# Kernel tuning notes

Hardware: AMD Instinct MI355X
Metric: run time of the kernel (lower is better)

The kernel has to match this reference:

```python
import jax, jax.numpy as jnp
import numpy as np

B, T, F, H = 1024, 128, 64, 256
HH = H // 2
A = 2  # action_space_size


def setup_inputs() -> dict:
    key = jax.random.key(0)
    ks = jax.random.split(key, 16)
    s = 0.05
    return {
        "history": jax.random.normal(ks[0], (B, T, F), jnp.float32),
        "head": jax.random.normal(ks[1], (B, 3), jnp.float32),
        # peephole LSTM params (TF LSTMCell gate order: i, j, f, o)
        "kernel": jax.random.normal(ks[2], (F + H, 4 * H), jnp.float32) * s,
        "bias": jnp.zeros((4 * H,), jnp.float32),
        "w_i": jax.random.normal(ks[3], (H,), jnp.float32) * s,
        "w_f": jax.random.normal(ks[4], (H,), jnp.float32) * s,
        "w_o": jax.random.normal(ks[5], (H,), jnp.float32) * s,
        # dueling heads
        "fc3_w": jax.random.normal(ks[6], (H + 2, HH), jnp.float32) * s,
        "fc3_b": jnp.zeros((HH,), jnp.float32),
        "fc4_w": jax.random.normal(ks[7], (H + 2, HH), jnp.float32) * s,
        "fc4_b": jnp.zeros((HH,), jnp.float32),
        "sell_v_w": jax.random.normal(ks[8], (HH, 1), jnp.float32) * s,
        "sell_v_b": jnp.zeros((1,), jnp.float32),
        "sell_q_w": jax.random.normal(ks[9], (HH, A), jnp.float32) * s,
        "sell_q_b": jnp.zeros((A,), jnp.float32),
        "buy_v_w": jax.random.normal(ks[10], (HH, 1), jnp.float32) * s,
        "buy_v_b": jnp.zeros((1,), jnp.float32),
        "buy_q_w": jax.random.normal(ks[11], (HH, A), jnp.float32) * s,
        "buy_q_b": jnp.zeros((A,), jnp.float32),
    }


def _peephole_lstm(history, kernel, bias, w_i, w_f, w_o):
    # history: [B, T, F] -> final hidden state h: [B, H]
    b = history.shape[0]
    h_dim = w_i.shape[0]
    xs = jnp.swapaxes(history, 0, 1)  # [T, B, F] time-major for scan
    c0 = jnp.zeros((b, h_dim), history.dtype)
    h0 = jnp.zeros((b, h_dim), history.dtype)

    def step(carry, x_t):
        c, h = carry
        z = jnp.concatenate([x_t, h], axis=-1) @ kernel + bias  # [B, 4H]
        i, j, f, o = jnp.split(z, 4, axis=-1)
        i = jax.nn.sigmoid(i + w_i * c)
        f = jax.nn.sigmoid(f + 1.0 + w_f * c)  # forget_bias = 1.0 (TF default)
        c_new = f * c + i * jnp.tanh(j)
        o = jax.nn.sigmoid(o + w_o * c_new)
        h_new = o * jnp.tanh(c_new)
        return (c_new, h_new), None

    (c_fin, h_fin), _ = jax.lax.scan(step, (c0, h0), xs)
    return h_fin


def reference(history, head, kernel, bias, w_i, w_f, w_o,
              fc3_w, fc3_b, fc4_w, fc4_b,
              sell_v_w, sell_v_b, sell_q_w, sell_q_b,
              buy_v_w, buy_v_b, buy_q_w, buy_q_b):
    state = _peephole_lstm(history, kernel, bias, w_i, w_f, w_o)  # [B, H]
    is_pos = head[:, :1]   # [B, 1]
    net_pnl = head[:, 1:]  # [B, 2]
    feature = jnp.concatenate([net_pnl, state], axis=-1)  # [B, H+2]

    value_logits = jax.nn.relu(feature @ fc3_w + fc3_b)
    q_logits = jax.nn.relu(feature @ fc4_w + fc4_b)

    pos_adv = q_logits @ sell_q_w + sell_q_b
    pos_q = pos_adv - jnp.mean(pos_adv, axis=-1, keepdims=True) + (value_logits @ sell_v_w + sell_v_b)
    emp_adv = q_logits @ buy_q_w + buy_q_b
    emp_q = emp_adv - jnp.mean(emp_adv, axis=-1, keepdims=True) + (value_logits @ buy_v_w + buy_v_b)

    mask = jnp.concatenate([is_pos, 1.0 - is_pos], axis=1).astype(bool)  # [B, 2]
    q = jnp.where(mask, pos_q, emp_q)
    return q
```

## Files before the change

kernel.cpp:

```cpp
#include <hip/hip_runtime.h>
#include <stdint.h>

#define B_TOTAL 1024
#define T_STEPS 128
#define F_DIM   64
#define H_DIM   256
#define BROWS   16
#define APAD    324
#define NSLOTS  640

typedef float f32x4 __attribute__((ext_vector_type(4)));
typedef short bf16x8 __attribute__((ext_vector_type(8)));

__device__ __forceinline__ unsigned short f2bf(float f) {
  unsigned int u = __float_as_uint(f);
  u += 0x7fffu + ((u >> 16) & 1u);
  return (unsigned short)(u >> 16);
}
__device__ __forceinline__ float bf2f(unsigned short b) {
  return __uint_as_float(((unsigned int)b) << 16);
}
__device__ __forceinline__ float sigmoid_f(float x) {
  return 1.0f / (1.0f + __expf(-x));
}
__device__ __forceinline__ float tanh_f(float x) {
  return 1.0f - 2.0f / (1.0f + __expf(2.0f * x));
}

__global__ __launch_bounds__(64) void pack_w_kernel(const float* __restrict__ W,
                                                    unsigned short* __restrict__ Wp) {
  const int slot = blockIdx.x;
  const int w  = slot / 80, r = slot % 80;
  const int kt = r >> 3, ct = (r >> 2) & 1, g = r & 3;
  const int ntile = g * 16 + w * 2 + ct;
  const int l   = threadIdx.x;
  const int col = ntile * 16 + (l & 15);
  const int k0  = kt * 32 + (l >> 4) * 8;
  unsigned short* dst = Wp + ((size_t)slot * 64 + l) * 8;
  #pragma unroll
  for (int j = 0; j < 8; ++j)
    dst[j] = f2bf(W[(size_t)(k0 + j) * 1024 + col]);
}

#define PIN(x) asm volatile("" : "+v"(x))

#define ISSUE_BATCH(buf, kt, ct) do {                                        \
    const unsigned short* _p = wp_wl + ((kt) * 8 + (ct) * 4) * 512;          \
    asm volatile("global_load_dwordx4 %0, %4, off\n\t"                       \
                 "global_load_dwordx4 %1, %4, off offset:1024\n\t"           \
                 "global_load_dwordx4 %2, %4, off offset:2048\n\t"           \
                 "global_load_dwordx4 %3, %4, off offset:3072"               \
                 : "=&v"(buf[0]), "=&v"(buf[1]), "=&v"(buf[2]), "=&v"(buf[3])\
                 : "v"(_p));                                                 \
  } while (0)

#define CONSUME(buf, ct, N) do {                                             \
    asm volatile("s_waitcnt vmcnt(" #N ")" ::: "memory");                    \
    __builtin_amdgcn_sched_barrier(0);                                       \
    acc[ct][0] = __builtin_amdgcn_mfma_f32_16x16x32_bf16(af, buf[0], acc[ct][0], 0, 0, 0); \
    acc[ct][1] = __builtin_amdgcn_mfma_f32_16x16x32_bf16(af, buf[1], acc[ct][1], 0, 0, 0); \
    acc[ct][2] = __builtin_amdgcn_mfma_f32_16x16x32_bf16(af, buf[2], acc[ct][2], 0, 0, 0); \
    acc[ct][3] = __builtin_amdgcn_mfma_f32_16x16x32_bf16(af, buf[3], acc[ct][3], 0, 0, 0); \
  } while (0)

#define LD_A(kt) (*(const bf16x8*)&A_lds[cl][(kt) * 32 + kg * 8])

__global__ __launch_bounds__(512, 1) void qlstm_kernel(
    const float* __restrict__ history, const float* __restrict__ head,
    const float* __restrict__ bias,
    const float* __restrict__ w_i, const float* __restrict__ w_f, const float* __restrict__ w_o,
    const unsigned short* __restrict__ Wp,
    const float* __restrict__ fc3_w, const float* __restrict__ fc3_b,
    const float* __restrict__ fc4_w, const float* __restrict__ fc4_b,
    const float* __restrict__ sell_v_w, const float* __restrict__ sell_v_b,
    const float* __restrict__ sell_q_w, const float* __restrict__ sell_q_b,
    const float* __restrict__ buy_v_w, const float* __restrict__ buy_v_b,
    const float* __restrict__ buy_q_w, const float* __restrict__ buy_q_b,
    float* __restrict__ out) {

  __shared__ unsigned short A_lds[BROWS][APAD];
  __shared__ float feat[BROWS][258];
  __shared__ float v_lds[BROWS][128];
  __shared__ float q_lds[BROWS][128];
  __shared__ float ispos_lds[BROWS];

  const int tid = threadIdx.x;
  const int w   = tid >> 6;
  const int l   = tid & 63;
  const int cl  = l & 15;
  const int kg  = l >> 4;
  const int rb  = blockIdx.x * BROWS;

  const unsigned short* wp_wl = Wp + (size_t)(w * 80) * 512 + l * 8;

  bf16x8 wreg[3][2][4];
  #pragma unroll
  for (int kt = 0; kt < 3; ++kt)
    #pragma unroll
    for (int ct = 0; ct < 2; ++ct)
      #pragma unroll
      for (int g = 0; g < 4; ++g) {
        wreg[kt][ct][g] = *(const bf16x8*)(wp_wl + (kt * 8 + ct * 4 + g) * 512);
        PIN(wreg[kt][ct][g]);
      }

  for (int i = tid; i < BROWS * APAD; i += 512)
    ((unsigned short*)A_lds)[i] = 0;
  __syncthreads();
  {
    const int r  = tid >> 5;
    const int f0 = (tid & 31) * 2;
    const float2 xv = *(const float2*)&history[((size_t)(rb + r) * T_STEPS + 0) * F_DIM + f0];
    *(unsigned int*)&A_lds[r][f0] =
        (unsigned int)f2bf(xv.x) | ((unsigned int)f2bf(xv.y) << 16);
  }

  float bias_r[2][4], wi_r[2], wf_r[2], wo_r[2];
  #pragma unroll
  for (int ct = 0; ct < 2; ++ct) {
    const int hc = (w * 2 + ct) * 16 + cl;
    wi_r[ct] = w_i[hc]; wf_r[ct] = w_f[hc]; wo_r[ct] = w_o[hc];
    #pragma unroll
    for (int g = 0; g < 4; ++g) bias_r[ct][g] = bias[g * 256 + hc];
  }

  float c_st[2][4];
  #pragma unroll
  for (int ct = 0; ct < 2; ++ct)
    #pragma unroll
    for (int q = 0; q < 4; ++q) c_st[ct][q] = 0.0f;

  __syncthreads();

  for (int t = 0; t < T_STEPS; ++t) {
    f32x4 acc[2][4];
    #pragma unroll
    for (int ct = 0; ct < 2; ++ct)
      #pragma unroll
      for (int g = 0; g < 4; ++g)
        acc[ct][g] = (f32x4){0.f, 0.f, 0.f, 0.f};

    float2 xv;
    const bool havex = (t + 1 < T_STEPS);
    if (havex) {
      const float* xp =
          &history[((size_t)(rb + (tid >> 5)) * T_STEPS + (t + 1)) * F_DIM + (tid & 31) * 2];
      asm volatile("global_load_dwordx2 %0, %1, off" : "=&v"(xv) : "v"(xp));
    }

    bf16x8 sA[4], sB[4], sC[4];
    ISSUE_BATCH(sA, 3, 0);
    ISSUE_BATCH(sB, 3, 1);
    ISSUE_BATCH(sC, 4, 0);

    #pragma unroll
    for (int kt = 0; kt < 3; ++kt) {
      const bf16x8 afr = LD_A(kt);
      #pragma unroll
      for (int ct = 0; ct < 2; ++ct)
        #pragma unroll
        for (int g = 0; g < 4; ++g)
          acc[ct][g] =
              __builtin_amdgcn_mfma_f32_16x16x32_bf16(afr, wreg[kt][ct][g], acc[ct][g], 0, 0, 0);
    }

    bf16x8 af;
    af = LD_A(3);
    CONSUME(sA, 0, 8); ISSUE_BATCH(sA, 4, 1);
    CONSUME(sB, 1, 8); ISSUE_BATCH(sB, 5, 0);
    af = LD_A(4);
    CONSUME(sC, 0, 8); ISSUE_BATCH(sC, 5, 1);
    CONSUME(sA, 1, 8); ISSUE_BATCH(sA, 6, 0);
    af = LD_A(5);
    CONSUME(sB, 0, 8); ISSUE_BATCH(sB, 6, 1);
    CONSUME(sC, 1, 8); ISSUE_BATCH(sC, 7, 0);
    af = LD_A(6);
    CONSUME(sA, 0, 8); ISSUE_BATCH(sA, 7, 1);
    CONSUME(sB, 1, 8); ISSUE_BATCH(sB, 8, 0);
    af = LD_A(7);
    CONSUME(sC, 0, 8); ISSUE_BATCH(sC, 8, 1);
    CONSUME(sA, 1, 8); ISSUE_BATCH(sA, 9, 0);
    af = LD_A(8);
    CONSUME(sB, 0, 8); ISSUE_BATCH(sB, 9, 1);
    CONSUME(sC, 1, 8);
    af = LD_A(9);
    CONSUME(sA, 0, 4);
    CONSUME(sB, 1, 0);

    float h_val[2][4];
    #pragma unroll
    for (int ct = 0; ct < 2; ++ct) {
      #pragma unroll
      for (int q = 0; q < 4; ++q) {
        const float c_old = c_st[ct][q];
        const float ig = sigmoid_f(acc[ct][0][q] + bias_r[ct][0] + wi_r[ct] * c_old);
        const float fg = sigmoid_f(acc[ct][2][q] + bias_r[ct][2] + 1.0f + wf_r[ct] * c_old);
        const float jg = tanh_f(acc[ct][1][q] + bias_r[ct][1]);
        const float c_new = fg * c_old + ig * jg;
        const float og = sigmoid_f(acc[ct][3][q] + bias_r[ct][3] + wo_r[ct] * c_new);
        c_st[ct][q] = c_new;
        h_val[ct][q] = og * tanh_f(c_new);
      }
    }

    __syncthreads();

    #pragma unroll
    for (int ct = 0; ct < 2; ++ct) {
      const int hc = (w * 2 + ct) * 16 + cl;
      #pragma unroll
      for (int q = 0; q < 4; ++q)
        A_lds[4 * kg + q][64 + hc] = f2bf(h_val[ct][q]);
    }
    if (havex) {
      const int r  = tid >> 5;
      const int f0 = (tid & 31) * 2;
      *(unsigned int*)&A_lds[r][f0] =
          (unsigned int)f2bf(xv.x) | ((unsigned int)f2bf(xv.y) << 16);
    }
    __syncthreads();
  }

  for (int i = tid; i < BROWS * H_DIM; i += 512) {
    const int r = i >> 8, hc = i & 255;
    feat[r][2 + hc] = bf2f(A_lds[r][64 + hc]);
  }
  if (tid < BROWS) {
    feat[tid][0] = head[(rb + tid) * 3 + 1];
    feat[tid][1] = head[(rb + tid) * 3 + 2];
    ispos_lds[tid] = head[(rb + tid) * 3 + 0];
  }
  __syncthreads();

  #pragma unroll
  for (int p = 0; p < 4; ++p) {
    const int idx = p * 512 + tid;
    const int r = idx >> 7, hh = idx & 127;
    float s3 = fc3_b[hh], s4 = fc4_b[hh];
    for (int k = 0; k < 258; ++k) {
      const float fv = feat[r][k];
      s3 += fv * fc3_w[k * 128 + hh];
      s4 += fv * fc4_w[k * 128 + hh];
    }
    v_lds[r][hh] = fmaxf(s3, 0.0f);
    q_lds[r][hh] = fmaxf(s4, 0.0f);
  }
  __syncthreads();

  if (tid < BROWS) {
    const int r = tid;
    float pa0 = sell_q_b[0], pa1 = sell_q_b[1];
    float ea0 = buy_q_b[0],  ea1 = buy_q_b[1];
    float sv = sell_v_b[0], bv = buy_v_b[0];
    for (int hh = 0; hh < 128; ++hh) {
      const float qv = q_lds[r][hh], vv = v_lds[r][hh];
      pa0 += qv * sell_q_w[hh * 2 + 0];
      pa1 += qv * sell_q_w[hh * 2 + 1];
      ea0 += qv * buy_q_w[hh * 2 + 0];
      ea1 += qv * buy_q_w[hh * 2 + 1];
      sv += vv * sell_v_w[hh];
      bv += vv * buy_v_w[hh];
    }
    const float pm = 0.5f * (pa0 + pa1), em = 0.5f * (ea0 + ea1);
    const float pq0 = pa0 - pm + sv, pq1 = pa1 - pm + sv;
    const float eq0 = ea0 - em + bv, eq1 = ea1 - em + bv;
    const float ip = ispos_lds[r];
    out[(size_t)(rb + r) * 2 + 0] = (ip != 0.0f) ? pq0 : eq0;
    out[(size_t)(rb + r) * 2 + 1] = ((1.0f - ip) != 0.0f) ? pq1 : eq1;
  }
}

extern "C" void kernel_launch(void* const* d_in, const int* in_sizes, int n_in,
                              void* d_out, int out_size, void* d_ws, size_t ws_size,
                              hipStream_t stream) {
  (void)in_sizes; (void)n_in; (void)out_size; (void)ws_size;
  const float* history  = (const float*)d_in[0];
  const float* head     = (const float*)d_in[1];
  const float* Wk       = (const float*)d_in[2];
  const float* bias     = (const float*)d_in[3];
  const float* w_i      = (const float*)d_in[4];
  const float* w_f      = (const float*)d_in[5];
  const float* w_o      = (const float*)d_in[6];
  const float* fc3_w    = (const float*)d_in[7];
  const float* fc3_b    = (const float*)d_in[8];
  const float* fc4_w    = (const float*)d_in[9];
  const float* fc4_b    = (const float*)d_in[10];
  const float* sell_v_w = (const float*)d_in[11];
  const float* sell_v_b = (const float*)d_in[12];
  const float* sell_q_w = (const float*)d_in[13];
  const float* sell_q_b = (const float*)d_in[14];
  const float* buy_v_w  = (const float*)d_in[15];
  const float* buy_v_b  = (const float*)d_in[16];
  const float* buy_q_w  = (const float*)d_in[17];
  const float* buy_q_b  = (const float*)d_in[18];

  unsigned short* Wp = (unsigned short*)d_ws;

  pack_w_kernel<<<NSLOTS, 64, 0, stream>>>(Wk, Wp);
  qlstm_kernel<<<B_TOTAL / BROWS, 512, 0, stream>>>(
      history, head, bias, w_i, w_f, w_o, Wp,
      fc3_w, fc3_b, fc4_w, fc4_b,
      sell_v_w, sell_v_b, sell_q_w, sell_q_b,
      buy_v_w, buy_v_b, buy_q_w, buy_q_b,
      (float*)d_out);
}
```

Baseline: 789.8 us.

## Stage two k-tiles of LSTM weights in LDS to cut per-step global loads

```diff
diff --git a/kernel.cpp b/kernel.cpp
--- a/kernel.cpp
+++ b/kernel.cpp
@@ -54,13 +54,14 @@
                  : "v"(_p));                                                 \
   } while (0)
 
-#define CONSUME(buf, ct, N) do {                                             \
+#define CONSUME_S(buf, ct, afv, N) do {                                      \
     asm volatile("s_waitcnt vmcnt(" #N ")" ::: "memory");                    \
     __builtin_amdgcn_sched_barrier(0);                                       \
-    acc[ct][0] = __builtin_amdgcn_mfma_f32_16x16x32_bf16(af, buf[0], acc[ct][0], 0, 0, 0); \
-    acc[ct][1] = __builtin_amdgcn_mfma_f32_16x16x32_bf16(af, buf[1], acc[ct][1], 0, 0, 0); \
-    acc[ct][2] = __builtin_amdgcn_mfma_f32_16x16x32_bf16(af, buf[2], acc[ct][2], 0, 0, 0); \
-    acc[ct][3] = __builtin_amdgcn_mfma_f32_16x16x32_bf16(af, buf[3], acc[ct][3], 0, 0, 0); \
+    acc[ct][0] = __builtin_amdgcn_mfma_f32_16x16x32_bf16(afv, buf[0], acc[ct][0], 0, 0, 0); \
+    acc[ct][1] = __builtin_amdgcn_mfma_f32_16x16x32_bf16(afv, buf[1], acc[ct][1], 0, 0, 0); \
+    acc[ct][2] = __builtin_amdgcn_mfma_f32_16x16x32_bf16(afv, buf[2], acc[ct][2], 0, 0, 0); \
+    acc[ct][3] = __builtin_amdgcn_mfma_f32_16x16x32_bf16(afv, buf[3], acc[ct][3], 0, 0, 0); \
+    __builtin_amdgcn_sched_barrier(0);                                       \
   } while (0)
 
 #define LD_A(kt) (*(const bf16x8*)&A_lds[cl][(kt) * 32 + kg * 8])
@@ -79,10 +80,7 @@
     float* __restrict__ out) {
 
   __shared__ unsigned short A_lds[BROWS][APAD];
-  __shared__ float feat[BROWS][258];
-  __shared__ float v_lds[BROWS][128];
-  __shared__ float q_lds[BROWS][128];
-  __shared__ float ispos_lds[BROWS];
+  __shared__ unsigned short W_lds[128 * 512];
 
   const int tid = threadIdx.x;
   const int w   = tid >> 6;
@@ -92,6 +90,14 @@
   const int rb  = blockIdx.x * BROWS;
 
   const unsigned short* wp_wl = Wp + (size_t)(w * 80) * 512 + l * 8;
+  const unsigned short* wl_l  = W_lds + (w * 16) * 512 + l * 8;
+
+  for (int i = tid; i < 128 * 64; i += 512) {
+    const int s = i >> 6, l2 = i & 63;
+    const int fsrc = (s >> 4) * 80 + 32 + (s & 15);
+    *(uint4*)&W_lds[((size_t)s * 64 + l2) * 8] =
+        *(const uint4*)&Wp[((size_t)fsrc * 64 + l2) * 8];
+  }
 
   bf16x8 wreg[3][2][4];
   #pragma unroll
@@ -110,9 +116,9 @@
   {
     const int r  = tid >> 5;
     const int f0 = (tid & 31) * 2;
-    const float2 xv = *(const float2*)&history[((size_t)(rb + r) * T_STEPS + 0) * F_DIM + f0];
+    const float2 xv0 = *(const float2*)&history[((size_t)(rb + r) * T_STEPS + 0) * F_DIM + f0];
     *(unsigned int*)&A_lds[r][f0] =
-        (unsigned int)f2bf(xv.x) | ((unsigned int)f2bf(xv.y) << 16);
+        (unsigned int)f2bf(xv0.x) | ((unsigned int)f2bf(xv0.y) << 16);
   }
 
   float bias_r[2][4], wi_r[2], wf_r[2], wo_r[2];
@@ -133,13 +139,6 @@
   __syncthreads();
 
   for (int t = 0; t < T_STEPS; ++t) {
-    f32x4 acc[2][4];
-    #pragma unroll
-    for (int ct = 0; ct < 2; ++ct)
-      #pragma unroll
-      for (int g = 0; g < 4; ++g)
-        acc[ct][g] = (f32x4){0.f, 0.f, 0.f, 0.f};
-
     float2 xv;
     const bool havex = (t + 1 < T_STEPS);
     if (havex) {
@@ -148,10 +147,17 @@
       asm volatile("global_load_dwordx2 %0, %1, off" : "=&v"(xv) : "v"(xp));
     }
 
+    f32x4 acc[2][4];
+    #pragma unroll
+    for (int ct = 0; ct < 2; ++ct)
+      #pragma unroll
+      for (int g = 0; g < 4; ++g)
+        acc[ct][g] = (f32x4){0.f, 0.f, 0.f, 0.f};
+
     bf16x8 sA[4], sB[4], sC[4];
     ISSUE_BATCH(sA, 3, 0);
     ISSUE_BATCH(sB, 3, 1);
-    ISSUE_BATCH(sC, 4, 0);
+    ISSUE_BATCH(sC, 6, 0);
 
     #pragma unroll
     for (int kt = 0; kt < 3; ++kt) {
@@ -164,28 +170,34 @@
               __builtin_amdgcn_mfma_f32_16x16x32_bf16(afr, wreg[kt][ct][g], acc[ct][g], 0, 0, 0);
     }
 
+    #pragma unroll
+    for (int kt = 4; kt < 6; ++kt) {
+      const bf16x8 afr = LD_A(kt);
+      #pragma unroll
+      for (int ct = 0; ct < 2; ++ct)
+        #pragma unroll
+        for (int g = 0; g < 4; ++g) {
+          const bf16x8 b = *(const bf16x8*)(wl_l + ((kt - 4) * 8 + ct * 4 + g) * 512);
+          acc[ct][g] = __builtin_amdgcn_mfma_f32_16x16x32_bf16(afr, b, acc[ct][g], 0, 0, 0);
+        }
+    }
+
     bf16x8 af;
     af = LD_A(3);
-    CONSUME(sA, 0, 8); ISSUE_BATCH(sA, 4, 1);
-    CONSUME(sB, 1, 8); ISSUE_BATCH(sB, 5, 0);
-    af = LD_A(4);
-    CONSUME(sC, 0, 8); ISSUE_BATCH(sC, 5, 1);
-    CONSUME(sA, 1, 8); ISSUE_BATCH(sA, 6, 0);
-    af = LD_A(5);
-    CONSUME(sB, 0, 8); ISSUE_BATCH(sB, 6, 1);
-    CONSUME(sC, 1, 8); ISSUE_BATCH(sC, 7, 0);
+    CONSUME_S(sA, 0, af, 8); ISSUE_BATCH(sA, 6, 1);
+    CONSUME_S(sB, 1, af, 8); ISSUE_BATCH(sB, 7, 0);
     af = LD_A(6);
-    CONSUME(sA, 0, 8); ISSUE_BATCH(sA, 7, 1);
-    CONSUME(sB, 1, 8); ISSUE_BATCH(sB, 8, 0);
+    CONSUME_S(sC, 0, af, 8); ISSUE_BATCH(sC, 7, 1);
+    CONSUME_S(sA, 1, af, 8); ISSUE_BATCH(sA, 8, 0);
     af = LD_A(7);
-    CONSUME(sC, 0, 8); ISSUE_BATCH(sC, 8, 1);
-    CONSUME(sA, 1, 8); ISSUE_BATCH(sA, 9, 0);
+    CONSUME_S(sB, 0, af, 8); ISSUE_BATCH(sB, 8, 1);
+    CONSUME_S(sC, 1, af, 8); ISSUE_BATCH(sC, 9, 0);
     af = LD_A(8);
-    CONSUME(sB, 0, 8); ISSUE_BATCH(sB, 9, 1);
-    CONSUME(sC, 1, 8);
+    CONSUME_S(sA, 0, af, 8); ISSUE_BATCH(sA, 9, 1);
+    CONSUME_S(sB, 1, af, 8);
     af = LD_A(9);
-    CONSUME(sA, 0, 4);
-    CONSUME(sB, 1, 0);
+    CONSUME_S(sC, 0, af, 4);
+    CONSUME_S(sA, 1, af, 0);
 
     float h_val[2][4];
     #pragma unroll
@@ -221,14 +233,23 @@
     __syncthreads();
   }
 
+  asm volatile("s_waitcnt vmcnt(0)" ::: "memory");
+  __builtin_amdgcn_sched_barrier(0);
+  __syncthreads();
+
+  float* feat  = (float*)W_lds;
+  float* v_l   = feat + BROWS * 258;
+  float* q_l   = v_l + BROWS * 128;
+  float* ispos = q_l + BROWS * 128;
+
   for (int i = tid; i < BROWS * H_DIM; i += 512) {
     const int r = i >> 8, hc = i & 255;
-    feat[r][2 + hc] = bf2f(A_lds[r][64 + hc]);
+    feat[r * 258 + 2 + hc] = bf2f(A_lds[r][64 + hc]);
   }
   if (tid < BROWS) {
-    feat[tid][0] = head[(rb + tid) * 3 + 1];
-    feat[tid][1] = head[(rb + tid) * 3 + 2];
-    ispos_lds[tid] = head[(rb + tid) * 3 + 0];
+    feat[tid * 258 + 0] = head[(rb + tid) * 3 + 1];
+    feat[tid * 258 + 1] = head[(rb + tid) * 3 + 2];
+    ispos[tid] = head[(rb + tid) * 3 + 0];
   }
   __syncthreads();
 
@@ -238,12 +259,12 @@
     const int r = idx >> 7, hh = idx & 127;
     float s3 = fc3_b[hh], s4 = fc4_b[hh];
     for (int k = 0; k < 258; ++k) {
-      const float fv = feat[r][k];
+      const float fv = feat[r * 258 + k];
       s3 += fv * fc3_w[k * 128 + hh];
       s4 += fv * fc4_w[k * 128 + hh];
     }
-    v_lds[r][hh] = fmaxf(s3, 0.0f);
-    q_lds[r][hh] = fmaxf(s4, 0.0f);
+    v_l[r * 128 + hh] = fmaxf(s3, 0.0f);
+    q_l[r * 128 + hh] = fmaxf(s4, 0.0f);
   }
   __syncthreads();
 
@@ -253,7 +274,7 @@
     float ea0 = buy_q_b[0],  ea1 = buy_q_b[1];
     float sv = sell_v_b[0], bv = buy_v_b[0];
     for (int hh = 0; hh < 128; ++hh) {
-      const float qv = q_lds[r][hh], vv = v_lds[r][hh];
+      const float qv = q_l[r * 128 + hh], vv = v_l[r * 128 + hh];
       pa0 += qv * sell_q_w[hh * 2 + 0];
       pa1 += qv * sell_q_w[hh * 2 + 1];
       ea0 += qv * buy_q_w[hh * 2 + 0];
@@ -264,7 +285,7 @@
     const float pm = 0.5f * (pa0 + pa1), em = 0.5f * (ea0 + ea1);
     const float pq0 = pa0 - pm + sv, pq1 = pa1 - pm + sv;
     const float eq0 = ea0 - em + bv, eq1 = ea1 - em + bv;
-    const float ip = ispos_lds[r];
+    const float ip = ispos[r];
     out[(size_t)(rb + r) * 2 + 0] = (ip != 0.0f) ? pq0 : eq0;
     out[(size_t)(rb + r) * 2 + 1] = ((1.0f - ip) != 0.0f) ? pq1 : eq1;
   }
```

Result: faster. 681.8 us (-13.7%).
